# Performance work log

Measured on AMD Instinct MI355X. Metric: run time of the kernel, lower is better.

The kernel has to match this reference:

```python
import jax, jax.numpy as jnp
import numpy as np

NUM_LAYERS = 4
D_MODEL = 128
D_STATE = 16
DELTA_RANK = 8


def setup_inputs() -> dict:
    key = jax.random.key(0)
    ks = jax.random.split(key, 10)
    d, N, dr, L_ = D_MODEL, D_STATE, DELTA_RANK, NUM_LAYERS
    B, R, T = 4, 32, 1024
    x = jax.random.normal(ks[0], (B, R, T), dtype=jnp.float32)

    def w(k, shape, fan_in):
        return jax.random.normal(k, shape, dtype=jnp.float32) / np.sqrt(fan_in).astype(np.float32)

    inp_w = w(ks[1], (d, 1), 1)
    inp_b = jnp.zeros((d,), jnp.float32)
    outp_w = w(ks[2], (1, d), d)
    outp_b = jnp.zeros((1,), jnp.float32)
    ln_g = jnp.ones((L_, d), jnp.float32)
    ln_b = jnp.zeros((L_, d), jnp.float32)
    in_w = w(ks[3], (L_, 2 * d, d), d)
    conv_w = w(ks[4], (L_, d, 3), 3)
    conv_b = jnp.zeros((L_, d), jnp.float32)
    xp_w = w(ks[5], (L_, dr + 2 * N, d), d)
    dp_w = w(ks[6], (L_, d, dr), dr)
    # delta_proj bias = log(dt), dt ~ loguniform(dt_min, dt_max)
    dt = jnp.exp(jax.random.uniform(ks[7], (L_, d), dtype=jnp.float32) * (np.log(0.1) - np.log(0.001)) + np.log(0.001))
    dp_b = jnp.log(dt)
    # A_log = Re(log(-0.5 + i*imag)) = 0.5*log(0.25 + imag^2)
    A_imag = np.arange(1, N + 1, dtype=np.float32) / (1.0 + 2.0 * np.arange(N, dtype=np.float32))
    A_row = 0.5 * np.log(0.25 + A_imag ** 2)
    A_log = jnp.asarray(np.broadcast_to(A_row, (L_, d, N)).copy(), jnp.float32)
    Dp = 0.1 * jnp.ones((L_, d), jnp.float32)
    out_w = w(ks[8], (L_, d, d), d)
    return dict(x=x, inp_w=inp_w, inp_b=inp_b, outp_w=outp_w, outp_b=outp_b,
                ln_g=ln_g, ln_b=ln_b, in_w=in_w, conv_w=conv_w, conv_b=conv_b,
                xp_w=xp_w, dp_w=dp_w, dp_b=dp_b, A_log=A_log, Dp=Dp, out_w=out_w)


def _layernorm(x, g, b):
    mu = jnp.mean(x, -1, keepdims=True)
    v = jnp.var(x, -1, keepdims=True)
    return (x - mu) * jax.lax.rsqrt(v + 1e-5) * g + b


def _selective_scan(u, delta, A_log, Bm, Cm, Dp):
    # u, delta: (Bt, L, d); Bm, Cm: (Bt, L, N); A_log: (d, N); Dp: (d,)
    Bt, L, d = u.shape
    N = A_log.shape[1]
    A = -jnp.exp(A_log)  # (d, N)

    def step(x_prev, inp):
        u_t, dt_t, B_t, C_t = inp  # (Bt,d),(Bt,d),(Bt,N),(Bt,N)
        dA = jnp.exp(dt_t[..., None] * A)                       # (Bt,d,N)
        dBu = dt_t[..., None] * B_t[:, None, :] * u_t[..., None]  # (Bt,d,N)
        x_new = dA * x_prev + dBu
        y_t = jnp.einsum('bdn,bn->bd', x_new, C_t)
        return x_new, y_t

    x0 = jnp.zeros((Bt, d, N), dtype=u.dtype)
    _, ys = jax.lax.scan(step, x0, (u.swapaxes(0, 1), delta.swapaxes(0, 1),
                                    Bm.swapaxes(0, 1), Cm.swapaxes(0, 1)))
    return ys.swapaxes(0, 1) + u * Dp  # (Bt, L, d)


def _block(h, ln_g, ln_b, in_w, conv_w, conv_b, xp_w, dp_w, dp_b, A_log, Dp, out_w):
    Bt, L, d = h.shape
    dr = dp_w.shape[1]
    N = A_log.shape[1]
    z = _layernorm(h, ln_g, ln_b)
    xr = z @ in_w.T                      # (Bt, L, 2d)
    xi, res = jnp.split(xr, 2, axis=-1)
    # depthwise causal conv, kernel=3 (torch pad=2 then crop [:L] == left-pad 2)
    xp = jnp.pad(xi, ((0, 0), (2, 0), (0, 0)))
    xc = (xp[:, 0:L] * conv_w[:, 0] + xp[:, 1:L + 1] * conv_w[:, 1]
          + xp[:, 2:L + 2] * conv_w[:, 2]) + conv_b
    xc = jax.nn.silu(xc)
    dbc = xc @ xp_w.T                    # (Bt, L, dr + 2N)
    dlt, Bm, Cm = jnp.split(dbc, [dr, dr + N], axis=-1)
    delta = jax.nn.softplus(dlt @ dp_w.T + dp_b)  # (Bt, L, d)
    y = _selective_scan(xc, delta, A_log, Bm, Cm, Dp)
    y = y * jax.nn.silu(res)
    return y @ out_w.T


def reference(x, inp_w, inp_b, outp_w, outp_b, ln_g, ln_b, in_w, conv_w, conv_b,
              xp_w, dp_w, dp_b, A_log, Dp, out_w):
    B, R, T = x.shape
    h = x.reshape(B * R, T, 1) @ inp_w.T + inp_b  # (B*R, T, d)
    for i in range(ln_g.shape[0]):
        h = _block(h, ln_g[i], ln_b[i], in_w[i], conv_w[i], conv_b[i], xp_w[i],
                   dp_w[i], dp_b[i], A_log[i], Dp[i], out_w[i]) + h
    out = (h @ outp_w.T + outp_b)[..., 0]  # (B*R, T)
    return out.reshape(B, R, T)
```

## Files before the change

### kernel.cpp

```cpp
#include <hip/hip_runtime.h>
#include <math.h>

#define D 128
#define NSTATE 16
#define DR 8
#define T_SEQ 1024
#define NTOK 131072
#define SEG 8
#define SEGLEN 128
#define CH 16
#define ZS 136
#define XRS2 132

typedef __attribute__((ext_vector_type(8))) short bf16x8;
typedef __attribute__((ext_vector_type(4))) float f32x4;

#define LOG2E 1.44269504088896340736f
#define LN2   0.69314718055994530942f

__device__ __forceinline__ float sigmoidf_(float x) {
    return __builtin_amdgcn_rcpf(1.0f + exp2f(-x * LOG2E));
}
__device__ __forceinline__ float softplusf_(float x) {
    float t = LN2 * __builtin_amdgcn_logf(1.0f + exp2f(x * LOG2E));
    return (x > 20.0f) ? x : t;
}
__device__ __forceinline__ short f2bf(float f) {
    union { float f; unsigned u; } v; v.f = f;
    unsigned r = v.u + 0x7FFFu + ((v.u >> 16) & 1u);
    return (short)(r >> 16);
}
__device__ __forceinline__ float bf2f(short s) {
    union { unsigned u; float f; } v; v.u = ((unsigned)(unsigned short)s) << 16;
    return v.f;
}


__global__ void k_prepw(const float* __restrict__ src, short* __restrict__ hi,
                        short* __restrict__ lo, int n) {
    int i = blockIdx.x * 256 + threadIdx.x;
    if (i < n) {
        float f = src[i];
        short hh = f2bf(f);
        hi[i] = hh;
        lo[i] = f2bf(f - bf2f(hh));
    }
}

__global__ void k_prepw_xp(const float* __restrict__ src, short* __restrict__ hi,
                           short* __restrict__ lo) {
    int i = blockIdx.x * 256 + threadIdx.x;
    if (i >= 4 * 48 * 128) return;
    int l = i / (48 * 128);
    int rem = i - l * 48 * 128;
    int j = rem >> 7, k = rem & 127;
    float f = (j < 40) ? src[(l * 40 + j) * 128 + k] : 0.f;
    short hh = f2bf(f);
    hi[i] = hh;
    lo[i] = f2bf(f - bf2f(hh));
}

__global__ void k_a2(const float* __restrict__ A_log, float* __restrict__ A2, int total) {
    int idx = blockIdx.x * blockDim.x + threadIdx.x;
    if (idx < total) A2[idx] = -__expf(A_log[idx]) * LOG2E;
}

__global__ void k_init_h(const float* __restrict__ x, const float* __restrict__ inp_w,
                         const float* __restrict__ inp_b, float* __restrict__ h) {
    int idx = blockIdx.x * blockDim.x + threadIdx.x;
    int tok = idx >> 7;
    int d = idx & 127;
    h[idx] = x[tok] * inp_w[d] + inp_b[d];
}

__global__ __launch_bounds__(256) void k_ln_inproj_conv(
    const float* __restrict__ h, const float* __restrict__ ln_g, const float* __restrict__ ln_b,
    const short* __restrict__ wh, const short* __restrict__ wl,
    const short* __restrict__ xph, const short* __restrict__ xpl,
    const float* __restrict__ conv_w, const float* __restrict__ conv_b,
    float* __restrict__ xc, float* __restrict__ res,
    float* __restrict__ bc, float* __restrict__ dlt)
{
    __shared__ __align__(16) short zsh[48 * ZS];
    __shared__ __align__(16) short zsl[48 * ZS];
    __shared__ __align__(16) float xr[34 * XRS2];
    const int tid = threadIdx.x;
    const int wv = tid >> 6, lane = tid & 63;
    const int tstart = blockIdx.x * 32;
    const int tin = tstart & (T_SEQ - 1);

    for (int r = wv; r < 34; r += 4) {
        int tr = tin + r - 2;
        if (tr < 0) {
            zsh[r * ZS + lane] = 0; zsh[r * ZS + lane + 64] = 0;
            zsl[r * ZS + lane] = 0; zsl[r * ZS + lane + 64] = 0;
            continue;
        }
        size_t row = (size_t)(tstart + r - 2) * D;
        float a = h[row + lane];
        float b = h[row + lane + 64];
        float s = a + b, ss = a * a + b * b;
        #pragma unroll
        for (int m = 1; m < 64; m <<= 1) { s += __shfl_xor(s, m); ss += __shfl_xor(ss, m); }
        float mu = s * (1.0f / 128.0f);
        float var = ss * (1.0f / 128.0f) - mu * mu;
        float rstd = rsqrtf(var + 1e-5f);
        float z0 = (a - mu) * rstd * ln_g[lane]      + ln_b[lane];
        float z1 = (b - mu) * rstd * ln_g[lane + 64] + ln_b[lane + 64];
        short h0 = f2bf(z0), h1 = f2bf(z1);
        zsh[r * ZS + lane]      = h0;
        zsh[r * ZS + lane + 64] = h1;
        zsl[r * ZS + lane]      = f2bf(z0 - bf2f(h0));
        zsl[r * ZS + lane + 64] = f2bf(z1 - bf2f(h1));
    }
    for (int i = tid; i < 14 * 128; i += 256) {
        int r = 34 + (i >> 7), c = i & 127;
        zsh[r * ZS + c] = 0;
        zsl[r * ZS + c] = 0;
    }

    const int colb = wv * 64 + (lane & 15);
    const int kb = (lane >> 4) * 8;
    bf16x8 bw[4][4];
    #pragma unroll
    for (int ct = 0; ct < 4; ++ct)
        #pragma unroll
        for (int kf = 0; kf < 4; ++kf)
            bw[ct][kf] = *(const bf16x8*)&wh[(colb + ct * 16) * 128 + kf * 32 + kb];
    __syncthreads();

    f32x4 acc[3][4];
    #pragma unroll
    for (int b = 0; b < 3; ++b)
        #pragma unroll
        for (int ct = 0; ct < 4; ++ct)
            acc[b][ct] = (f32x4){0.f, 0.f, 0.f, 0.f};

    #pragma unroll
    for (int b = 0; b < 3; ++b) {
        bf16x8 ah[4], al[4];
        const int rbase = (b * 16 + (lane & 15)) * ZS + kb;
        #pragma unroll
        for (int kf = 0; kf < 4; ++kf) {
            ah[kf] = *(const bf16x8*)&zsh[rbase + kf * 32];
            al[kf] = *(const bf16x8*)&zsl[rbase + kf * 32];
        }
        #pragma unroll
        for (int ct = 0; ct < 4; ++ct)
            #pragma unroll
            for (int kf = 0; kf < 4; ++kf) {
                acc[b][ct] = __builtin_amdgcn_mfma_f32_16x16x32_bf16(ah[kf], bw[ct][kf], acc[b][ct], 0, 0, 0);
                acc[b][ct] = __builtin_amdgcn_mfma_f32_16x16x32_bf16(al[kf], bw[ct][kf], acc[b][ct], 0, 0, 0);
            }
    }
    #pragma unroll
    for (int ct = 0; ct < 4; ++ct)
        #pragma unroll
        for (int kf = 0; kf < 4; ++kf)
            bw[ct][kf] = *(const bf16x8*)&wl[(colb + ct * 16) * 128 + kf * 32 + kb];
    #pragma unroll
    for (int b = 0; b < 3; ++b) {
        bf16x8 ah[4];
        const int rbase = (b * 16 + (lane & 15)) * ZS + kb;
        #pragma unroll
        for (int kf = 0; kf < 4; ++kf)
            ah[kf] = *(const bf16x8*)&zsh[rbase + kf * 32];
        #pragma unroll
        for (int ct = 0; ct < 4; ++ct)
            #pragma unroll
            for (int kf = 0; kf < 4; ++kf)
                acc[b][ct] = __builtin_amdgcn_mfma_f32_16x16x32_bf16(ah[kf], bw[ct][kf], acc[b][ct], 0, 0, 0);
    }

    if (wv < 2) {
        #pragma unroll
        for (int b = 0; b < 3; ++b)
            #pragma unroll
            for (int ct = 0; ct < 4; ++ct) {
                const int col = wv * 64 + ct * 16 + (lane & 15);
                #pragma unroll
                for (int i = 0; i < 4; ++i) {
                    int row = b * 16 + ((lane >> 4) << 2) + i;
                    if (row < 34) xr[row * XRS2 + col] = acc[b][ct][i];
                }
            }
    } else {
        #pragma unroll
        for (int b = 0; b < 3; ++b)
            #pragma unroll
            for (int ct = 0; ct < 4; ++ct) {
                const int col = (wv - 2) * 64 + ct * 16 + (lane & 15);
                #pragma unroll
                for (int i = 0; i < 4; ++i) {
                    int row = b * 16 + ((lane >> 4) << 2) + i;
                    if (row >= 2 && row < 34)
                        res[(size_t)(tstart + row - 2) * D + col] = acc[b][ct][i];
                }
            }
    }
    __syncthreads();

    if (tid < 128) {
        float c0 = conv_w[tid * 3 + 0], c1 = conv_w[tid * 3 + 1], c2 = conv_w[tid * 3 + 2];
        float cb = conv_b[tid];
        float v0 = xr[0 * XRS2 + tid], v1 = xr[1 * XRS2 + tid];
        #pragma unroll
        for (int s = 0; s < 32; ++s) {
            float v2 = xr[(s + 2) * XRS2 + tid];
            float v = v0 * c0 + v1 * c1 + v2 * c2 + cb;
            v = v * sigmoidf_(v);
            xc[(size_t)(tstart + s) * D + tid] = v;
            short hh = f2bf(v);
            zsh[s * ZS + tid] = hh;
            zsl[s * ZS + tid] = f2bf(v - bf2f(hh));
            v0 = v1; v1 = v2;
        }
    }
    __syncthreads();

    for (int tile = wv; tile < 6; tile += 4) {
        const int b = tile & 1, ct = tile >> 1;
        const int jcol = ct * 16 + (lane & 15);
        const int rbase = (b * 16 + (lane & 15)) * ZS + kb;
        bf16x8 ah[4], al[4], bh[4];
        #pragma unroll
        for (int kf = 0; kf < 4; ++kf) {
            ah[kf] = *(const bf16x8*)&zsh[rbase + kf * 32];
            al[kf] = *(const bf16x8*)&zsl[rbase + kf * 32];
            bh[kf] = *(const bf16x8*)&xph[jcol * 128 + kf * 32 + kb];
        }
        f32x4 a2 = (f32x4){0.f, 0.f, 0.f, 0.f};
        #pragma unroll
        for (int kf = 0; kf < 4; ++kf) {
            a2 = __builtin_amdgcn_mfma_f32_16x16x32_bf16(ah[kf], bh[kf], a2, 0, 0, 0);
            a2 = __builtin_amdgcn_mfma_f32_16x16x32_bf16(al[kf], bh[kf], a2, 0, 0, 0);
        }
        #pragma unroll
        for (int kf = 0; kf < 4; ++kf) {
            bh[kf] = *(const bf16x8*)&xpl[jcol * 128 + kf * 32 + kb];
            a2 = __builtin_amdgcn_mfma_f32_16x16x32_bf16(ah[kf], bh[kf], a2, 0, 0, 0);
        }
        #pragma unroll
        for (int i = 0; i < 4; ++i) {
            int tok = tstart + b * 16 + ((lane >> 4) << 2) + i;
            if (jcol < 8)
                dlt[(size_t)tok * 8 + jcol] = a2[i];
            else if (jcol < 40)
                bc[(size_t)tok * 32 + (jcol - 8)] = a2[i];
        }
    }
}

__global__ __launch_bounds__(256) void k_scan1(
    const float* __restrict__ xc, const float* __restrict__ bc,
    const float* __restrict__ dlt,
    const float* __restrict__ dp_w, const float* __restrict__ dp_b,
    const float* __restrict__ A2,
    float* __restrict__ Pbuf, float* __restrict__ Fbuf)
{
    __shared__ float u_l[CH][64];
    __shared__ float du_l[CH][64];
    __shared__ float bc_l[CH][16];
    __shared__ float dlt_l[CH][8];
    __shared__ float dl_l[CH][64];
    __shared__ float dpw_s[64][9];
    __shared__ float dpb_s[64];

    const int tid = threadIdx.x;
    const int bt = blockIdx.x >> 4;
    const int seg = (blockIdx.x >> 1) & 7;
    const int d0 = (blockIdx.x & 1) * 64;
    const int dd = tid >> 2, q = tid & 3;
    const int d = d0 + dd;

    #pragma unroll
    for (int i = 0; i < 2; ++i) {
        int idx = tid + i * 256;
        dpw_s[idx >> 3][idx & 7] = dp_w[(d0 + (idx >> 3)) * 8 + (idx & 7)];
    }
    if (tid < 64) dpb_s[tid] = dp_b[d0 + tid];
    float A2q[4];
    #pragma unroll
    for (int jn = 0; jn < 4; ++jn) A2q[jn] = A2[d * NSTATE + q * 4 + jn];
    float x0 = 0.f, x1 = 0.f, x2 = 0.f, x3 = 0.f, S = 0.f;

    const size_t segbase = (size_t)bt * T_SEQ + (size_t)seg * SEGLEN;
    float4 su, sbc, sdl;
    su = *(const float4*)&xc[(segbase + (tid >> 4)) * D + d0 + (tid & 15) * 4];
    if (tid < 64)  sbc = *(const float4*)&bc[(segbase + (tid >> 2)) * 32 + (tid & 3) * 4];
    if (tid < 32)  sdl = *(const float4*)&dlt[(segbase + (tid >> 1)) * 8 + (tid & 1) * 4];

    for (int c = 0; c < SEGLEN / CH; ++c) {
        *(float4*)&u_l[tid >> 4][(tid & 15) * 4] = su;
        if (tid < 64)  *(float4*)&bc_l[tid >> 2][(tid & 3) * 4] = sbc;
        if (tid < 32)  *(float4*)&dlt_l[tid >> 1][(tid & 1) * 4] = sdl;
        __syncthreads();
        if (c + 1 < SEGLEN / CH) {
            const size_t nb = segbase + (size_t)(c + 1) * CH;
            su = *(const float4*)&xc[(nb + (tid >> 4)) * D + d0 + (tid & 15) * 4];
            if (tid < 64)  sbc = *(const float4*)&bc[(nb + (tid >> 2)) * 32 + (tid & 3) * 4];
            if (tid < 32)  sdl = *(const float4*)&dlt[(nb + (tid >> 1)) * 8 + (tid & 1) * 4];
        }
        {
            int col = tid & 63;
            #pragma unroll
            for (int i = 0; i < 4; ++i) {
                int row = (tid >> 6) + 4 * i;
                float v = dpb_s[col];
                #pragma unroll
                for (int r = 0; r < DR; ++r) v = fmaf(dlt_l[row][r], dpw_s[col][r], v);
                float dt = softplusf_(v);
                dl_l[row][col] = dt;
                du_l[row][col] = dt * u_l[row][col];
            }
        }
        __syncthreads();
        #pragma unroll
        for (int tl = 0; tl < CH; ++tl) {
            float dt = dl_l[tl][dd];
            float duv = du_l[tl][dd];
            S += dt;
            float4 Bq = *(const float4*)&bc_l[tl][q * 4];
            x0 = fmaf(exp2f(dt * A2q[0]), x0, duv * Bq.x);
            x1 = fmaf(exp2f(dt * A2q[1]), x1, duv * Bq.y);
            x2 = fmaf(exp2f(dt * A2q[2]), x2, duv * Bq.z);
            x3 = fmaf(exp2f(dt * A2q[3]), x3, duv * Bq.w);
        }
        __syncthreads();
    }
    const size_t o = ((size_t)(bt * SEG + seg) * D + d) * NSTATE + q * 4;
    *(float4*)&Fbuf[o] = make_float4(x0, x1, x2, x3);
    *(float4*)&Pbuf[o] = make_float4(exp2f(A2q[0] * S), exp2f(A2q[1] * S),
                                     exp2f(A2q[2] * S), exp2f(A2q[3] * S));
}

__global__ __launch_bounds__(256) void k_scan2(
    const float* __restrict__ xc, const float* __restrict__ bc,
    const float* __restrict__ dlt,
    const float* __restrict__ dp_w, const float* __restrict__ dp_b,
    const float* __restrict__ A2, const float* __restrict__ Dp,
    const float* __restrict__ Pbuf, const float* __restrict__ Fbuf,
    float* __restrict__ resy)
{
    __shared__ float u_l[CH][64];
    __shared__ float r_l[CH][64];
    __shared__ float bc_l[CH][32];
    __shared__ float dlt_l[CH][8];
    __shared__ float dl_l[CH][64];
    __shared__ float dpw_s[64][9];
    __shared__ float dpb_s[64];

    const int tid = threadIdx.x;
    const int bt = blockIdx.x >> 4;
    const int seg = (blockIdx.x >> 1) & 7;
    const int d0 = (blockIdx.x & 1) * 64;
    const int dd = tid >> 2, q = tid & 3;
    const int d = d0 + dd;

    #pragma unroll
    for (int i = 0; i < 2; ++i) {
        int idx = tid + i * 256;
        dpw_s[idx >> 3][idx & 7] = dp_w[(d0 + (idx >> 3)) * 8 + (idx & 7)];
    }
    if (tid < 64) dpb_s[tid] = dp_b[d0 + tid];
    float A2q[4];
    #pragma unroll
    for (int jn = 0; jn < 4; ++jn) A2q[jn] = A2[d * NSTATE + q * 4 + jn];
    const float Dpd = Dp[d];

    float x0 = 0.f, x1 = 0.f, x2 = 0.f, x3 = 0.f;
    for (int s = 0; s < seg; ++s) {
        const size_t idx = ((size_t)(bt * SEG + s) * D + d) * NSTATE + q * 4;
        float4 P = *(const float4*)&Pbuf[idx];
        float4 F = *(const float4*)&Fbuf[idx];
        x0 = fmaf(P.x, x0, F.x);
        x1 = fmaf(P.y, x1, F.y);
        x2 = fmaf(P.z, x2, F.z);
        x3 = fmaf(P.w, x3, F.w);
    }

    const size_t segbase = (size_t)bt * T_SEQ + (size_t)seg * SEGLEN;
    float4 su, sr, sbc, sdl;
    su = *(const float4*)&xc[(segbase + (tid >> 4)) * D + d0 + (tid & 15) * 4];
    sr = *(const float4*)&resy[(segbase + (tid >> 4)) * D + d0 + (tid & 15) * 4];
    if (tid < 128) sbc = *(const float4*)&bc[(segbase + (tid >> 3)) * 32 + (tid & 7) * 4];
    if (tid < 32)  sdl = *(const float4*)&dlt[(segbase + (tid >> 1)) * 8 + (tid & 1) * 4];

    for (int c = 0; c < SEGLEN / CH; ++c) {
        const size_t tb = segbase + (size_t)c * CH;
        *(float4*)&u_l[tid >> 4][(tid & 15) * 4] = su;
        *(float4*)&r_l[tid >> 4][(tid & 15) * 4] = sr;
        if (tid < 128) *(float4*)&bc_l[tid >> 3][(tid & 7) * 4] = sbc;
        if (tid < 32)  *(float4*)&dlt_l[tid >> 1][(tid & 1) * 4] = sdl;
        __syncthreads();
        if (c + 1 < SEGLEN / CH) {
            const size_t nb = tb + CH;
            su = *(const float4*)&xc[(nb + (tid >> 4)) * D + d0 + (tid & 15) * 4];
            sr = *(const float4*)&resy[(nb + (tid >> 4)) * D + d0 + (tid & 15) * 4];
            if (tid < 128) sbc = *(const float4*)&bc[(nb + (tid >> 3)) * 32 + (tid & 7) * 4];
            if (tid < 32)  sdl = *(const float4*)&dlt[(nb + (tid >> 1)) * 8 + (tid & 1) * 4];
        }
        {
            int col = tid & 63;
            #pragma unroll
            for (int i = 0; i < 4; ++i) {
                int row = (tid >> 6) + 4 * i;
                float v = dpb_s[col];
                #pragma unroll
                for (int r = 0; r < DR; ++r) v = fmaf(dlt_l[row][r], dpw_s[col][r], v);
                dl_l[row][col] = softplusf_(v);
            }
        }
        __syncthreads();
        float pacc[CH];
        #pragma unroll
        for (int tl = 0; tl < CH; ++tl) {
            float dt = dl_l[tl][dd];
            float uv = u_l[tl][dd];
            float duv = dt * uv;
            float4 Bq = *(const float4*)&bc_l[tl][q * 4];
            float4 Cq = *(const float4*)&bc_l[tl][16 + q * 4];
            x0 = fmaf(exp2f(dt * A2q[0]), x0, duv * Bq.x);
            x1 = fmaf(exp2f(dt * A2q[1]), x1, duv * Bq.y);
            x2 = fmaf(exp2f(dt * A2q[2]), x2, duv * Bq.z);
            x3 = fmaf(exp2f(dt * A2q[3]), x3, duv * Bq.w);
            float p = x0 * Cq.x;
            p = fmaf(x1, Cq.y, p);
            p = fmaf(x2, Cq.z, p);
            p = fmaf(x3, Cq.w, p);
            p += __shfl_xor(p, 1);
            p += __shfl_xor(p, 2);
            pacc[tl] = fmaf(uv, Dpd, p);
        }
        if (q == 0) {
            #pragma unroll
            for (int tl = 0; tl < CH; ++tl) {
                float g = r_l[tl][dd];
                resy[(tb + tl) * D + d] = pacc[tl] * (g * sigmoidf_(g));
            }
        }
        __syncthreads();
    }
}

__global__ __launch_bounds__(256) void k_outproj(
    const float* __restrict__ y, const short* __restrict__ wh, const short* __restrict__ wl,
    float* __restrict__ h)
{
    __shared__ __align__(16) short ysh[32 * ZS];
    __shared__ __align__(16) short ysl[32 * ZS];
    const int tid = threadIdx.x;
    const int wv = tid >> 6, lane = tid & 63;
    const size_t tb = (size_t)blockIdx.x * 32;

    #pragma unroll
    for (int i = 0; i < 4; ++i) {
        int idx = tid + i * 256;
        int row = idx >> 5, c4 = idx & 31;
        float4 v = *(const float4*)&y[(tb + row) * D + c4 * 4];
        short h0 = f2bf(v.x), h1 = f2bf(v.y), h2 = f2bf(v.z), h3 = f2bf(v.w);
        *(short4*)&ysh[row * ZS + c4 * 4] = make_short4(h0, h1, h2, h3);
        *(short4*)&ysl[row * ZS + c4 * 4] = make_short4(
            f2bf(v.x - bf2f(h0)), f2bf(v.y - bf2f(h1)),
            f2bf(v.z - bf2f(h2)), f2bf(v.w - bf2f(h3)));
    }

    const int colb = wv * 32 + (lane & 15);
    const int kb = (lane >> 4) * 8;
    bf16x8 bw[2][4];
    #pragma unroll
    for (int ct = 0; ct < 2; ++ct)
        #pragma unroll
        for (int kf = 0; kf < 4; ++kf)
            bw[ct][kf] = *(const bf16x8*)&wh[(colb + ct * 16) * 128 + kf * 32 + kb];
    __syncthreads();

    f32x4 acc[2][2];
    #pragma unroll
    for (int b = 0; b < 2; ++b)
        #pragma unroll
        for (int ct = 0; ct < 2; ++ct)
            acc[b][ct] = (f32x4){0.f, 0.f, 0.f, 0.f};

    #pragma unroll
    for (int b = 0; b < 2; ++b) {
        bf16x8 ah[4], al[4];
        const int rbase = (b * 16 + (lane & 15)) * ZS + kb;
        #pragma unroll
        for (int kf = 0; kf < 4; ++kf) {
            ah[kf] = *(const bf16x8*)&ysh[rbase + kf * 32];
            al[kf] = *(const bf16x8*)&ysl[rbase + kf * 32];
        }
        #pragma unroll
        for (int ct = 0; ct < 2; ++ct)
            #pragma unroll
            for (int kf = 0; kf < 4; ++kf) {
                acc[b][ct] = __builtin_amdgcn_mfma_f32_16x16x32_bf16(ah[kf], bw[ct][kf], acc[b][ct], 0, 0, 0);
                acc[b][ct] = __builtin_amdgcn_mfma_f32_16x16x32_bf16(al[kf], bw[ct][kf], acc[b][ct], 0, 0, 0);
            }
    }
    #pragma unroll
    for (int ct = 0; ct < 2; ++ct)
        #pragma unroll
        for (int kf = 0; kf < 4; ++kf)
            bw[ct][kf] = *(const bf16x8*)&wl[(colb + ct * 16) * 128 + kf * 32 + kb];
    #pragma unroll
    for (int b = 0; b < 2; ++b) {
        bf16x8 ah[4];
        const int rbase = (b * 16 + (lane & 15)) * ZS + kb;
        #pragma unroll
        for (int kf = 0; kf < 4; ++kf)
            ah[kf] = *(const bf16x8*)&ysh[rbase + kf * 32];
        #pragma unroll
        for (int ct = 0; ct < 2; ++ct)
            #pragma unroll
            for (int kf = 0; kf < 4; ++kf)
                acc[b][ct] = __builtin_amdgcn_mfma_f32_16x16x32_bf16(ah[kf], bw[ct][kf], acc[b][ct], 0, 0, 0);
    }

    #pragma unroll
    for (int b = 0; b < 2; ++b)
        #pragma unroll
        for (int ct = 0; ct < 2; ++ct) {
            const int col = wv * 32 + ct * 16 + (lane & 15);
            #pragma unroll
            for (int i = 0; i < 4; ++i) {
                int row = b * 16 + ((lane >> 4) << 2) + i;
                size_t o = (tb + row) * D + col;
                h[o] += acc[b][ct][i];
            }
        }
}

__global__ __launch_bounds__(256) void k_final(
    const float* __restrict__ h, const float* __restrict__ outp_w,
    const float* __restrict__ outp_b, float* __restrict__ out)
{
    const int tid = threadIdx.x;
    const int lane = tid & 63;
    const size_t tok = (size_t)blockIdx.x * 4 + (tid >> 6);
    float a = h[tok * D + lane] * outp_w[lane] + h[tok * D + lane + 64] * outp_w[lane + 64];
    #pragma unroll
    for (int m = 1; m < 64; m <<= 1) a += __shfl_xor(a, m);
    if (lane == 0) out[tok] = a + outp_b[0];
}

extern "C" void kernel_launch(void* const* d_in, const int* in_sizes, int n_in,
                              void* d_out, int out_size, void* d_ws, size_t ws_size,
                              hipStream_t stream)
{
    const float* x      = (const float*)d_in[0];
    const float* inp_w  = (const float*)d_in[1];
    const float* inp_b  = (const float*)d_in[2];
    const float* outp_w = (const float*)d_in[3];
    const float* outp_b = (const float*)d_in[4];
    const float* ln_g   = (const float*)d_in[5];
    const float* ln_b   = (const float*)d_in[6];
    const float* in_w   = (const float*)d_in[7];
    const float* conv_w = (const float*)d_in[8];
    const float* conv_b = (const float*)d_in[9];
    const float* xp_w   = (const float*)d_in[10];
    const float* dp_w   = (const float*)d_in[11];
    const float* dp_b   = (const float*)d_in[12];
    const float* A_log  = (const float*)d_in[13];
    const float* Dp     = (const float*)d_in[14];
    const float* out_w  = (const float*)d_in[15];

    float* ws = (float*)d_ws;
    size_t off = 0;
    float* h      = ws + off; off += (size_t)NTOK * D;
    float* xc     = ws + off; off += (size_t)NTOK * D;
    float* resy   = ws + off; off += (size_t)NTOK * D;
    float* bc     = ws + off; off += (size_t)NTOK * 32;
    float* dlt    = ws + off; off += (size_t)NTOK * 8;
    float* Pbuf   = ws + off; off += 128 * SEG * 2048;
    float* Fbuf   = ws + off; off += 128 * SEG * 2048;
    short* in_wBh = (short*)(ws + off); off += 4 * 256 * 128 / 2;
    short* in_wBl = (short*)(ws + off); off += 4 * 256 * 128 / 2;
    short* out_wBh= (short*)(ws + off); off += 4 * 128 * 128 / 2;
    short* out_wBl= (short*)(ws + off); off += 4 * 128 * 128 / 2;
    short* xp_wBh = (short*)(ws + off); off += 4 * 48 * 128 / 2;
    short* xp_wBl = (short*)(ws + off); off += 4 * 48 * 128 / 2;
    float* A2     = ws + off; off += 4 * 128 * 16;
    if (ws_size < off * sizeof(float)) return;

    k_prepw<<<(4 * 256 * 128 + 255) / 256, 256, 0, stream>>>(in_w, in_wBh, in_wBl, 4 * 256 * 128);
    k_prepw<<<(4 * 128 * 128 + 255) / 256, 256, 0, stream>>>(out_w, out_wBh, out_wBl, 4 * 128 * 128);
    k_prepw_xp<<<(4 * 48 * 128 + 255) / 256, 256, 0, stream>>>(xp_w, xp_wBh, xp_wBl);
    k_a2<<<(4 * 128 * 16 + 255) / 256, 256, 0, stream>>>(A_log, A2, 4 * 128 * 16);
    k_init_h<<<NTOK * D / 256, 256, 0, stream>>>(x, inp_w, inp_b, h);

    for (int l = 0; l < 4; ++l) {
        k_ln_inproj_conv<<<NTOK / 32, 256, 0, stream>>>(
            h, ln_g + l * 128, ln_b + l * 128,
            in_wBh + l * 256 * 128, in_wBl + l * 256 * 128,
            xp_wBh + l * 48 * 128, xp_wBl + l * 48 * 128,
            conv_w + l * 128 * 3, conv_b + l * 128, xc, resy, bc, dlt);
        k_scan1<<<2048, 256, 0, stream>>>(xc, bc, dlt, dp_w + l * 128 * 8, dp_b + l * 128,
                                          A2 + l * 128 * 16, Pbuf, Fbuf);
        k_scan2<<<2048, 256, 0, stream>>>(xc, bc, dlt, dp_w + l * 128 * 8, dp_b + l * 128,
                                          A2 + l * 128 * 16, Dp + l * 128, Pbuf, Fbuf, resy);
        k_outproj<<<NTOK / 32, 256, 0, stream>>>(resy, out_wBh + l * 128 * 128,
                                                 out_wBl + l * 128 * 128, h);
    }
    k_final<<<NTOK / 4, 256, 0, stream>>>(h, outp_w, outp_b, (float*)d_out);
}
```

Measured before the change: 1.531 ms.

## Restructure chunked scan: local-output pass then cross-segment correction pass

The first scan pass now computes each segment's local output from a zero initial state, including the C contraction and the D skip term. It writes that output in place over xc and also produces the segment carry factors. The second pass no longer re-runs the recurrence. It adds the contribution of the incoming state through the cumulative sum of dt, exp2(A*S_t)*x_in contracted with C, then applies the silu gate. This removes the serial per-step recurrence and the B loads from the second pass. In exchange it adds a prefix sum and exponentials per step, and it overwrites the xc buffer.

```diff
diff --git a/kernel.cpp b/kernel.cpp
--- a/kernel.cpp
+++ b/kernel.cpp
@@ -251,16 +251,15 @@
     }
 }
 
-__global__ __launch_bounds__(256) void k_scan1(
-    const float* __restrict__ xc, const float* __restrict__ bc,
-    const float* __restrict__ dlt,
+__global__ __launch_bounds__(256) void k_scanA(
+    float* __restrict__ xcy,
+    const float* __restrict__ bc, const float* __restrict__ dlt,
     const float* __restrict__ dp_w, const float* __restrict__ dp_b,
-    const float* __restrict__ A2,
+    const float* __restrict__ A2, const float* __restrict__ Dp,
     float* __restrict__ Pbuf, float* __restrict__ Fbuf)
 {
     __shared__ float u_l[CH][64];
-    __shared__ float du_l[CH][64];
-    __shared__ float bc_l[CH][16];
+    __shared__ float bc_l[CH][32];
     __shared__ float dlt_l[CH][8];
     __shared__ float dl_l[CH][64];
     __shared__ float dpw_s[64][9];
@@ -282,121 +281,24 @@
     float A2q[4];
     #pragma unroll
     for (int jn = 0; jn < 4; ++jn) A2q[jn] = A2[d * NSTATE + q * 4 + jn];
+    const float Dpd = Dp[d];
     float x0 = 0.f, x1 = 0.f, x2 = 0.f, x3 = 0.f, S = 0.f;
 
     const size_t segbase = (size_t)bt * T_SEQ + (size_t)seg * SEGLEN;
     float4 su, sbc, sdl;
-    su = *(const float4*)&xc[(segbase + (tid >> 4)) * D + d0 + (tid & 15) * 4];
-    if (tid < 64)  sbc = *(const float4*)&bc[(segbase + (tid >> 2)) * 32 + (tid & 3) * 4];
-    if (tid < 32)  sdl = *(const float4*)&dlt[(segbase + (tid >> 1)) * 8 + (tid & 1) * 4];
-
-    for (int c = 0; c < SEGLEN / CH; ++c) {
-        *(float4*)&u_l[tid >> 4][(tid & 15) * 4] = su;
-        if (tid < 64)  *(float4*)&bc_l[tid >> 2][(tid & 3) * 4] = sbc;
-        if (tid < 32)  *(float4*)&dlt_l[tid >> 1][(tid & 1) * 4] = sdl;
-        __syncthreads();
-        if (c + 1 < SEGLEN / CH) {
-            const size_t nb = segbase + (size_t)(c + 1) * CH;
-            su = *(const float4*)&xc[(nb + (tid >> 4)) * D + d0 + (tid & 15) * 4];
-            if (tid < 64)  sbc = *(const float4*)&bc[(nb + (tid >> 2)) * 32 + (tid & 3) * 4];
-            if (tid < 32)  sdl = *(const float4*)&dlt[(nb + (tid >> 1)) * 8 + (tid & 1) * 4];
-        }
-        {
-            int col = tid & 63;
-            #pragma unroll
-            for (int i = 0; i < 4; ++i) {
-                int row = (tid >> 6) + 4 * i;
-                float v = dpb_s[col];
-                #pragma unroll
-                for (int r = 0; r < DR; ++r) v = fmaf(dlt_l[row][r], dpw_s[col][r], v);
-                float dt = softplusf_(v);
-                dl_l[row][col] = dt;
-                du_l[row][col] = dt * u_l[row][col];
-            }
-        }
-        __syncthreads();
-        #pragma unroll
-        for (int tl = 0; tl < CH; ++tl) {
-            float dt = dl_l[tl][dd];
-            float duv = du_l[tl][dd];
-            S += dt;
-            float4 Bq = *(const float4*)&bc_l[tl][q * 4];
-            x0 = fmaf(exp2f(dt * A2q[0]), x0, duv * Bq.x);
-            x1 = fmaf(exp2f(dt * A2q[1]), x1, duv * Bq.y);
-            x2 = fmaf(exp2f(dt * A2q[2]), x2, duv * Bq.z);
-            x3 = fmaf(exp2f(dt * A2q[3]), x3, duv * Bq.w);
-        }
-        __syncthreads();
-    }
-    const size_t o = ((size_t)(bt * SEG + seg) * D + d) * NSTATE + q * 4;
-    *(float4*)&Fbuf[o] = make_float4(x0, x1, x2, x3);
-    *(float4*)&Pbuf[o] = make_float4(exp2f(A2q[0] * S), exp2f(A2q[1] * S),
-                                     exp2f(A2q[2] * S), exp2f(A2q[3] * S));
-}
-
-__global__ __launch_bounds__(256) void k_scan2(
-    const float* __restrict__ xc, const float* __restrict__ bc,
-    const float* __restrict__ dlt,
-    const float* __restrict__ dp_w, const float* __restrict__ dp_b,
-    const float* __restrict__ A2, const float* __restrict__ Dp,
-    const float* __restrict__ Pbuf, const float* __restrict__ Fbuf,
-    float* __restrict__ resy)
-{
-    __shared__ float u_l[CH][64];
-    __shared__ float r_l[CH][64];
-    __shared__ float bc_l[CH][32];
-    __shared__ float dlt_l[CH][8];
-    __shared__ float dl_l[CH][64];
-    __shared__ float dpw_s[64][9];
-    __shared__ float dpb_s[64];
-
-    const int tid = threadIdx.x;
-    const int bt = blockIdx.x >> 4;
-    const int seg = (blockIdx.x >> 1) & 7;
-    const int d0 = (blockIdx.x & 1) * 64;
-    const int dd = tid >> 2, q = tid & 3;
-    const int d = d0 + dd;
-
-    #pragma unroll
-    for (int i = 0; i < 2; ++i) {
-        int idx = tid + i * 256;
-        dpw_s[idx >> 3][idx & 7] = dp_w[(d0 + (idx >> 3)) * 8 + (idx & 7)];
-    }
-    if (tid < 64) dpb_s[tid] = dp_b[d0 + tid];
-    float A2q[4];
-    #pragma unroll
-    for (int jn = 0; jn < 4; ++jn) A2q[jn] = A2[d * NSTATE + q * 4 + jn];
-    const float Dpd = Dp[d];
-
-    float x0 = 0.f, x1 = 0.f, x2 = 0.f, x3 = 0.f;
-    for (int s = 0; s < seg; ++s) {
-        const size_t idx = ((size_t)(bt * SEG + s) * D + d) * NSTATE + q * 4;
-        float4 P = *(const float4*)&Pbuf[idx];
-        float4 F = *(const float4*)&Fbuf[idx];
-        x0 = fmaf(P.x, x0, F.x);
-        x1 = fmaf(P.y, x1, F.y);
-        x2 = fmaf(P.z, x2, F.z);
-        x3 = fmaf(P.w, x3, F.w);
-    }
-
-    const size_t segbase = (size_t)bt * T_SEQ + (size_t)seg * SEGLEN;
-    float4 su, sr, sbc, sdl;
-    su = *(const float4*)&xc[(segbase + (tid >> 4)) * D + d0 + (tid & 15) * 4];
-    sr = *(const float4*)&resy[(segbase + (tid >> 4)) * D + d0 + (tid & 15) * 4];
+    su = *(const float4*)&xcy[(segbase + (tid >> 4)) * D + d0 + (tid & 15) * 4];
     if (tid < 128) sbc = *(const float4*)&bc[(segbase + (tid >> 3)) * 32 + (tid & 7) * 4];
     if (tid < 32)  sdl = *(const float4*)&dlt[(segbase + (tid >> 1)) * 8 + (tid & 1) * 4];
 
     for (int c = 0; c < SEGLEN / CH; ++c) {
         const size_t tb = segbase + (size_t)c * CH;
         *(float4*)&u_l[tid >> 4][(tid & 15) * 4] = su;
-        *(float4*)&r_l[tid >> 4][(tid & 15) * 4] = sr;
         if (tid < 128) *(float4*)&bc_l[tid >> 3][(tid & 7) * 4] = sbc;
         if (tid < 32)  *(float4*)&dlt_l[tid >> 1][(tid & 1) * 4] = sdl;
         __syncthreads();
         if (c + 1 < SEGLEN / CH) {
             const size_t nb = tb + CH;
-            su = *(const float4*)&xc[(nb + (tid >> 4)) * D + d0 + (tid & 15) * 4];
-            sr = *(const float4*)&resy[(nb + (tid >> 4)) * D + d0 + (tid & 15) * 4];
+            su = *(const float4*)&xcy[(nb + (tid >> 4)) * D + d0 + (tid & 15) * 4];
             if (tid < 128) sbc = *(const float4*)&bc[(nb + (tid >> 3)) * 32 + (tid & 7) * 4];
             if (tid < 32)  sdl = *(const float4*)&dlt[(nb + (tid >> 1)) * 8 + (tid & 1) * 4];
         }
@@ -418,6 +320,7 @@
             float dt = dl_l[tl][dd];
             float uv = u_l[tl][dd];
             float duv = dt * uv;
+            S += dt;
             float4 Bq = *(const float4*)&bc_l[tl][q * 4];
             float4 Cq = *(const float4*)&bc_l[tl][16 + q * 4];
             x0 = fmaf(exp2f(dt * A2q[0]), x0, duv * Bq.x);
@@ -434,9 +337,121 @@
         }
         if (q == 0) {
             #pragma unroll
+            for (int tl = 0; tl < CH; ++tl)
+                xcy[(tb + tl) * D + d] = pacc[tl];
+        }
+        __syncthreads();
+    }
+    const size_t o = ((size_t)(bt * SEG + seg) * D + d) * NSTATE + q * 4;
+    *(float4*)&Fbuf[o] = make_float4(x0, x1, x2, x3);
+    *(float4*)&Pbuf[o] = make_float4(exp2f(A2q[0] * S), exp2f(A2q[1] * S),
+                                     exp2f(A2q[2] * S), exp2f(A2q[3] * S));
+}
+
+__global__ __launch_bounds__(256) void k_scanB(
+    const float* __restrict__ ylocal,
+    const float* __restrict__ bc, const float* __restrict__ dlt,
+    const float* __restrict__ dp_w, const float* __restrict__ dp_b,
+    const float* __restrict__ A2,
+    const float* __restrict__ Pbuf, const float* __restrict__ Fbuf,
+    float* __restrict__ resy)
+{
+    __shared__ float yl_l[CH][64];
+    __shared__ float r_l[CH][64];
+    __shared__ float c_l[CH][16];
+    __shared__ float dlt_l[CH][8];
+    __shared__ float dl_l[CH][64];
+    __shared__ float dpw_s[64][9];
+    __shared__ float dpb_s[64];
+
+    const int tid = threadIdx.x;
+    const int bt = blockIdx.x >> 4;
+    const int seg = (blockIdx.x >> 1) & 7;
+    const int d0 = (blockIdx.x & 1) * 64;
+    const int dd = tid >> 2, q = tid & 3;
+    const int d = d0 + dd;
+
+    #pragma unroll
+    for (int i = 0; i < 2; ++i) {
+        int idx = tid + i * 256;
+        dpw_s[idx >> 3][idx & 7] = dp_w[(d0 + (idx >> 3)) * 8 + (idx & 7)];
+    }
+    if (tid < 64) dpb_s[tid] = dp_b[d0 + tid];
+    float A2q[4];
+    #pragma unroll
+    for (int jn = 0; jn < 4; ++jn) A2q[jn] = A2[d * NSTATE + q * 4 + jn];
+
+    float xi0 = 0.f, xi1 = 0.f, xi2 = 0.f, xi3 = 0.f;
+    for (int s = 0; s < seg; ++s) {
+        const size_t idx = ((size_t)(bt * SEG + s) * D + d) * NSTATE + q * 4;
+        float4 P = *(const float4*)&Pbuf[idx];
+        float4 F = *(const float4*)&Fbuf[idx];
+        xi0 = fmaf(P.x, xi0, F.x);
+        xi1 = fmaf(P.y, xi1, F.y);
+        xi2 = fmaf(P.z, xi2, F.z);
+        xi3 = fmaf(P.w, xi3, F.w);
+    }
+
+    const size_t segbase = (size_t)bt * T_SEQ + (size_t)seg * SEGLEN;
+    float S = 0.f;
+    float4 sy, sr, sc, sdl;
+    sy = *(const float4*)&ylocal[(segbase + (tid >> 4)) * D + d0 + (tid & 15) * 4];
+    sr = *(const float4*)&resy[(segbase + (tid >> 4)) * D + d0 + (tid & 15) * 4];
+    if (tid < 64) sc = *(const float4*)&bc[(segbase + (tid >> 2)) * 32 + 16 + (tid & 3) * 4];
+    if (tid < 32) sdl = *(const float4*)&dlt[(segbase + (tid >> 1)) * 8 + (tid & 1) * 4];
+
+    for (int c = 0; c < SEGLEN / CH; ++c) {
+        const size_t tb = segbase + (size_t)c * CH;
+        *(float4*)&yl_l[tid >> 4][(tid & 15) * 4] = sy;
+        *(float4*)&r_l[tid >> 4][(tid & 15) * 4] = sr;
+        if (tid < 64) *(float4*)&c_l[tid >> 2][(tid & 3) * 4] = sc;
+        if (tid < 32) *(float4*)&dlt_l[tid >> 1][(tid & 1) * 4] = sdl;
+        __syncthreads();
+        if (c + 1 < SEGLEN / CH) {
+            const size_t nb = tb + CH;
+            sy = *(const float4*)&ylocal[(nb + (tid >> 4)) * D + d0 + (tid & 15) * 4];
+            sr = *(const float4*)&resy[(nb + (tid >> 4)) * D + d0 + (tid & 15) * 4];
+            if (tid < 64) sc = *(const float4*)&bc[(nb + (tid >> 2)) * 32 + 16 + (tid & 3) * 4];
+            if (tid < 32) sdl = *(const float4*)&dlt[(nb + (tid >> 1)) * 8 + (tid & 1) * 4];
+        }
+        {
+            int col = tid & 63;
+            #pragma unroll
+            for (int i = 0; i < 4; ++i) {
+                int row = (tid >> 6) + 4 * i;
+                float v = dpb_s[col];
+                #pragma unroll
+                for (int r = 0; r < DR; ++r) v = fmaf(dlt_l[row][r], dpw_s[col][r], v);
+                dl_l[row][col] = softplusf_(v);
+            }
+        }
+        __syncthreads();
+        float Sv[CH];
+        {
+            float s = S;
+            #pragma unroll
+            for (int tl = 0; tl < CH; ++tl) { s += dl_l[tl][dd]; Sv[tl] = s; }
+            S = s;
+        }
+        float pacc[CH];
+        #pragma unroll
+        for (int tl = 0; tl < CH; ++tl) {
+            float4 Cq = *(const float4*)&c_l[tl][q * 4];
+            float p;
+            p = (exp2f(A2q[0] * Sv[tl]) * xi0) * Cq.x;
+            p = fmaf(exp2f(A2q[1] * Sv[tl]) * xi1, Cq.y, p);
+            p = fmaf(exp2f(A2q[2] * Sv[tl]) * xi2, Cq.z, p);
+            p = fmaf(exp2f(A2q[3] * Sv[tl]) * xi3, Cq.w, p);
+            p += __shfl_xor(p, 1);
+            p += __shfl_xor(p, 2);
+            pacc[tl] = p;
+        }
+        if (q == 0) {
+            #pragma unroll
             for (int tl = 0; tl < CH; ++tl) {
                 float g = r_l[tl][dd];
-                resy[(tb + tl) * D + d] = pacc[tl] * (g * sigmoidf_(g));
+                float y = yl_l[tl][dd] + pacc[tl];
+                resy[(tb + tl) * D + d] = y * (g * sigmoidf_(g));
             }
         }
         __syncthreads();
@@ -596,10 +611,10 @@
             in_wBh + l * 256 * 128, in_wBl + l * 256 * 128,
             xp_wBh + l * 48 * 128, xp_wBl + l * 48 * 128,
             conv_w + l * 128 * 3, conv_b + l * 128, xc, resy, bc, dlt);
-        k_scan1<<<2048, 256, 0, stream>>>(xc, bc, dlt, dp_w + l * 128 * 8, dp_b + l * 128,
-                                          A2 + l * 128 * 16, Pbuf, Fbuf);
-        k_scan2<<<2048, 256, 0, stream>>>(xc, bc, dlt, dp_w + l * 128 * 8, dp_b + l * 128,
-                                          A2 + l * 128 * 16, Dp + l * 128, Pbuf, Fbuf, resy);
+        k_scanA<<<2048, 256, 0, stream>>>(xc, bc, dlt, dp_w + l * 128 * 8, dp_b + l * 128,
+                                          A2 + l * 128 * 16, Dp + l * 128, Pbuf, Fbuf);
+        k_scanB<<<2048, 256, 0, stream>>>(xc, bc, dlt, dp_w + l * 128 * 8, dp_b + l * 128,
+                                          A2 + l * 128 * 16, Pbuf, Fbuf, resy);
         k_outproj<<<NTOK / 32, 256, 0, stream>>>(resy, out_wBh + l * 128 * 128,
                                                  out_wBl + l * 128 * 128, h);
     }
```

Result: slower. 1.572 ms (+2.6%).
